# Kernel tuning notes

Hardware: AMD Instinct MI355X
Metric: run time of the kernel (lower is better)

Reference implementation:

```python
import jax, jax.numpy as jnp
import numpy as np

MAX_HOPS = 3


def setup_inputs() -> dict:
    key = jax.random.key(0)
    ks = jax.random.split(key, 6)
    B, M, S = 128, 200, 20
    V, D = 100000, 128
    NC, CL = 10000, 10
    stories = jax.random.randint(ks[0], (B, M, S), 0, V, dtype=jnp.int64)
    queries = jax.random.randint(ks[1], (B, S), 0, V, dtype=jnp.int64)
    candidates = jax.random.randint(ks[2], (NC, CL), 0, V, dtype=jnp.int64)
    # 0.05 scale keeps hop softmax logits in a sane range
    A_tab = jax.random.normal(ks[3], (V, D), dtype=jnp.float32) * 0.05
    W_tab = jax.random.normal(ks[4], (V, D), dtype=jnp.float32) * 0.05
    H_w = jax.random.normal(ks[5], (D, D), dtype=jnp.float32) * 0.05
    return {"stories": stories, "queries": queries, "candidates": candidates,
            "A_tab": A_tab, "W_tab": W_tab, "H_w": H_w}


def reference(stories, queries, candidates, A_tab, W_tab, H_w):
    # padding_idx=0: embedding row 0 is zero
    A = A_tab.at[0].set(0.0)
    W = W_tab.at[0].set(0.0)
    # query encoding: gather + sum-pool -> [B, D]
    u = jnp.sum(A[queries], axis=1)
    # memory encoding: [B, M, D] (same A table each hop, as in the source)
    m = jnp.sum(A[stories], axis=2)
    for _ in range(MAX_HOPS):
        dotted = jnp.einsum('bmd,bd->bm', m, u)          # attention logits
        probs = jax.nn.softmax(dotted, axis=1)           # [B, M]
        o = jnp.einsum('bm,bmd->bd', probs, m)           # weighted memory sum
        u = jnp.tanh(u @ H_w.T + o)                      # Linear(no bias) + tanh
    cand_sum = jnp.sum(W[candidates], axis=1)            # [NC, D]
    logits = u @ cand_sum.T                              # [B, NC]
    return logits
```

## Files before the change

kernel.cpp:

```cpp
#include <hip/hip_runtime.h>
#include <hip/hip_bf16.h>
#include <math.h>

#define BB 128
#define MM 200
#define SS 20
#define DD 128
#define NC 10000
#define CL 10
#define LCT 64
#define NROW (BB * MM)
#define GS_BLK (NROW / 16)
#define GQ_BLK (BB / 16)
#define GC_BLK (NC / 8)

__device__ __forceinline__ unsigned pack_bf16(float a, float b) {
    unsigned ua = __float_as_uint(a), ub = __float_as_uint(b);
    ua += 0x7fff + ((ua >> 16) & 1);
    ub += 0x7fff + ((ub >> 16) & 1);
    return (ua >> 16) | (ub & 0xffff0000u);
}
__device__ __forceinline__ float bflo(unsigned v) { return __uint_as_float(v << 16); }
__device__ __forceinline__ float bfhi(unsigned v) { return __uint_as_float(v & 0xffff0000u); }

__device__ __forceinline__ int detect_shift(const int* __restrict__ q) {
    int zc = 0;
#pragma unroll
    for (int i = 0; i < 8; ++i) zc += (q[2 * i + 1] == 0);
    return (zc >= 6) ? 1 : 0;
}

__global__ __launch_bounds__(512) void k_conv(const float* __restrict__ A,
                                              unsigned* __restrict__ Abf) {
    size_t t = (size_t)blockIdx.x * 512 + threadIdx.x;
    const float4* in = (const float4*)(A + t * 8);
    float4 a = in[0], b = in[1];
    if (t * 8 < DD) {
        a = make_float4(0.f, 0.f, 0.f, 0.f);
        b = make_float4(0.f, 0.f, 0.f, 0.f);
    }
    uint4 o;
    o.x = pack_bf16(a.x, a.y);
    o.y = pack_bf16(a.z, a.w);
    o.z = pack_bf16(b.x, b.y);
    o.w = pack_bf16(b.z, b.w);
    ((uint4*)(Abf + t * 4))[0] = o;
}

__global__ __launch_bounds__(256) void k_gather(const int* __restrict__ stories,
                                                const int* __restrict__ queries,
                                                const int* __restrict__ cands,
                                                const unsigned* __restrict__ Abf,
                                                const float* __restrict__ W,
                                                unsigned* __restrict__ m_all,
                                                float* __restrict__ u0_all,
                                                float* __restrict__ cand_buf) {
    int bid = blockIdx.x;
    int tid = threadIdx.x;
    int shift = detect_shift(queries);

    if (bid < GS_BLK) {
        int g = tid >> 4, l = tid & 15;
        int r = bid * 16 + g;
        int toks[SS];
#pragma unroll
        for (int s = 0; s < SS; ++s)
            toks[s] = stories[((size_t)(r * SS + s)) << shift];
        float a[8] = {0.f, 0.f, 0.f, 0.f, 0.f, 0.f, 0.f, 0.f};
#pragma unroll
        for (int s = 0; s < SS; ++s) {
            uint4 v = ((const uint4*)(Abf + ((size_t)(unsigned)toks[s] << 6)))[l];
            a[0] += bflo(v.x); a[1] += bfhi(v.x);
            a[2] += bflo(v.y); a[3] += bfhi(v.y);
            a[4] += bflo(v.z); a[5] += bfhi(v.z);
            a[6] += bflo(v.w); a[7] += bfhi(v.w);
        }
        uint4 o;
        o.x = pack_bf16(a[0], a[1]);
        o.y = pack_bf16(a[2], a[3]);
        o.z = pack_bf16(a[4], a[5]);
        o.w = pack_bf16(a[6], a[7]);
        ((uint4*)(m_all + (size_t)r * (DD / 2)))[l] = o;
    } else if (bid < GS_BLK + GQ_BLK) {
        int g = tid >> 4, l = tid & 15;
        int b = (bid - GS_BLK) * 16 + g;
        int toks[SS];
#pragma unroll
        for (int s = 0; s < SS; ++s)
            toks[s] = queries[((size_t)(b * SS + s)) << shift];
        float a[8] = {0.f, 0.f, 0.f, 0.f, 0.f, 0.f, 0.f, 0.f};
#pragma unroll
        for (int s = 0; s < SS; ++s) {
            uint4 v = ((const uint4*)(Abf + ((size_t)(unsigned)toks[s] << 6)))[l];
            a[0] += bflo(v.x); a[1] += bfhi(v.x);
            a[2] += bflo(v.y); a[3] += bfhi(v.y);
            a[4] += bflo(v.z); a[5] += bfhi(v.z);
            a[6] += bflo(v.w); a[7] += bfhi(v.w);
        }
        float4* op = (float4*)(u0_all + (size_t)b * DD + l * 8);
        op[0] = make_float4(a[0], a[1], a[2], a[3]);
        op[1] = make_float4(a[4], a[5], a[6], a[7]);
    } else {
        int g = tid >> 5, l = tid & 31;
        int row = (bid - GS_BLK - GQ_BLK) * 8 + g;
        int toks[CL];
#pragma unroll
        for (int s = 0; s < CL; ++s)
            toks[s] = cands[((size_t)(row * CL + s)) << shift];
        float4 acc = make_float4(0.f, 0.f, 0.f, 0.f);
#pragma unroll
        for (int s = 0; s < CL; ++s) {
            float4 v = ((const float4*)(W + (size_t)(unsigned)toks[s] * DD))[l];
            float msk = toks[s] ? 1.f : 0.f;
            acc.x = fmaf(msk, v.x, acc.x);
            acc.y = fmaf(msk, v.y, acc.y);
            acc.z = fmaf(msk, v.z, acc.z);
            acc.w = fmaf(msk, v.w, acc.w);
        }
        ((float4*)(cand_buf + (size_t)row * DD))[l] = acc;
    }
}

__global__ __launch_bounds__(512) void k_hops(const unsigned* __restrict__ m_all,
                                              const float* __restrict__ u0_all,
                                              const float* __restrict__ Hw,
                                              float* __restrict__ uT) {
    __shared__ unsigned m_s[MM][DD / 2];
    __shared__ float u_s[DD];
    __shared__ float p_s[MM];
    __shared__ float o_part[8][DD];
    __shared__ float red_s;

    int b = blockIdx.x;
    int tid = threadIdx.x;

    {
        const uint4* src = (const uint4*)(m_all + (size_t)b * MM * (DD / 2));
        uint4* dst = (uint4*)&m_s[0][0];
        for (int i = tid; i < MM * (DD / 2) / 4; i += 512) dst[i] = src[i];
    }
    if (tid < DD) u_s[tid] = u0_all[(size_t)b * DD + tid];
    __syncthreads();

    for (int hop = 0; hop < 3; ++hop) {
        if (tid < MM) {
            const float2* u2 = (const float2*)u_s;
            float acc = 0.f;
#pragma unroll 8
            for (int li = 0; li < 64; ++li) {
                int j = (tid + li) & 63;
                unsigned pv = m_s[tid][j];
                float2 uv = u2[j];
                acc += bflo(pv) * uv.x + bfhi(pv) * uv.y;
            }
            p_s[tid] = acc;
        }
        __syncthreads();
        if (tid < 64) {
            float v0 = p_s[tid], v1 = p_s[tid + 64], v2 = p_s[tid + 128];
            float v3 = (tid < 8) ? p_s[tid + 192] : -1e30f;
            float mx = fmaxf(fmaxf(v0, v1), fmaxf(v2, v3));
            for (int off = 32; off; off >>= 1) mx = fmaxf(mx, __shfl_down(mx, off));
            mx = __shfl(mx, 0);
            float e0 = __expf(v0 - mx), e1 = __expf(v1 - mx), e2 = __expf(v2 - mx);
            float e3 = (tid < 8) ? __expf(v3 - mx) : 0.f;
            float sm = e0 + e1 + e2 + e3;
            for (int off = 32; off; off >>= 1) sm += __shfl_down(sm, off);
            p_s[tid] = e0;
            p_s[tid + 64] = e1;
            p_s[tid + 128] = e2;
            if (tid < 8) p_s[tid + 192] = e3;
            if (tid == 0) red_s = 1.f / __shfl(sm, 0);
        }
        __syncthreads();
        {
            int c = tid & 63, h = tid >> 6;
            int mm0 = h * 25;
            float ax = 0.f, ay = 0.f;
#pragma unroll 5
            for (int k = 0; k < 25; ++k) {
                unsigned pv = m_s[mm0 + k][c];
                float p = p_s[mm0 + k];
                ax = fmaf(p, bflo(pv), ax);
                ay = fmaf(p, bfhi(pv), ay);
            }
            o_part[h][2 * c] = ax;
            o_part[h][2 * c + 1] = ay;
        }
        __syncthreads();
        float u_new = 0.f;
        if (tid < DD) {
            float o = 0.f;
#pragma unroll
            for (int h = 0; h < 8; ++h) o += o_part[h][tid];
            float acc = o * red_s;
            const float4* hrow = (const float4*)(Hw + tid * DD);
            const float4* u4 = (const float4*)u_s;
#pragma unroll 8
            for (int j = 0; j < DD / 4; ++j) {
                float4 hv = hrow[j];
                float4 uv = u4[j];
                acc += hv.x * uv.x + hv.y * uv.y + hv.z * uv.z + hv.w * uv.w;
            }
            u_new = tanhf(acc);
        }
        __syncthreads();
        if (tid < DD) u_s[tid] = u_new;
        __syncthreads();
    }
    if (tid < DD) uT[tid * BB + b] = u_s[tid];
}

__global__ __launch_bounds__(256) void k_logits(const float* __restrict__ uT,
                                                const float* __restrict__ cs,
                                                float* __restrict__ out) {
    __shared__ float c_s[DD][LCT + 4];
    int c0 = blockIdx.x * LCT;
    int tid = threadIdx.x;
    {
        int c = tid >> 2, l = tid & 3;
        int row = c0 + c;
        if (row >= NC) row = NC - 1;
        const float4* rp = (const float4*)(cs + (size_t)row * DD);
#pragma unroll
        for (int i = 0; i < 8; ++i) {
            int k = (l << 5) + (i << 2);
            float4 v = rp[(l << 3) + i];
            c_s[k][c] = v.x;
            c_s[k + 1][c] = v.y;
            c_s[k + 2][c] = v.z;
            c_s[k + 3][c] = v.w;
        }
    }
    __syncthreads();
    int tx = tid & 31, ty = tid >> 5;
    const float* cb = &c_s[0][ty << 3];
    const float4* up = (const float4*)(uT + (tx << 2));
    float acc[4][8];
#pragma unroll
    for (int i = 0; i < 4; ++i)
#pragma unroll
        for (int j = 0; j < 8; ++j) acc[i][j] = 0.f;
#pragma unroll 4
    for (int k = 0; k < DD; ++k) {
        float4 uv = up[k * (BB / 4)];
        float4 ca = *(const float4*)(cb + k * (LCT + 4));
        float4 cc = *(const float4*)(cb + k * (LCT + 4) + 4);
        float uu[4] = {uv.x, uv.y, uv.z, uv.w};
        float cv[8] = {ca.x, ca.y, ca.z, ca.w, cc.x, cc.y, cc.z, cc.w};
#pragma unroll
        for (int i = 0; i < 4; ++i)
#pragma unroll
            for (int j = 0; j < 8; ++j) acc[i][j] = fmaf(uu[i], cv[j], acc[i][j]);
    }
    if (c0 + (ty << 3) < NC) {
#pragma unroll
        for (int i = 0; i < 4; ++i) {
            float* orow = out + (size_t)((tx << 2) + i) * NC + c0 + (ty << 3);
            ((float4*)orow)[0] = make_float4(acc[i][0], acc[i][1], acc[i][2], acc[i][3]);
            ((float4*)orow)[1] = make_float4(acc[i][4], acc[i][5], acc[i][6], acc[i][7]);
        }
    }
}

extern "C" void kernel_launch(void* const* d_in, const int* in_sizes, int n_in,
                              void* d_out, int out_size, void* d_ws, size_t ws_size,
                              hipStream_t stream) {
    const int* stories = (const int*)d_in[0];
    const int* queries = (const int*)d_in[1];
    const int* cands   = (const int*)d_in[2];
    const float* A  = (const float*)d_in[3];
    const float* W  = (const float*)d_in[4];
    const float* Hw = (const float*)d_in[5];
    float* out = (float*)d_out;

    unsigned* Abf = (unsigned*)d_ws;
    float* cand_buf = (float*)(Abf + (size_t)100000 * (DD / 2));
    float* uT_buf = cand_buf + (size_t)NC * DD;
    float* u0_buf = uT_buf + (size_t)BB * DD;
    unsigned* m_all = (unsigned*)(u0_buf + (size_t)BB * DD);

    k_conv<<<100000 * DD / 8 / 512, 512, 0, stream>>>(A, Abf);
    k_gather<<<GS_BLK + GQ_BLK + GC_BLK, 256, 0, stream>>>(stories, queries, cands,
                                                           Abf, W, m_all, u0_buf,
                                                           cand_buf);
    k_hops<<<BB, 512, 0, stream>>>(m_all, u0_buf, Hw, uT_buf);
    k_logits<<<(NC + LCT - 1) / LCT, 256, 0, stream>>>(uT_buf, cand_buf, out);
}
```

Baseline: 189.1 us.

## Quantize A table to int8 with per-row scales for story gather

```diff
diff --git a/kernel.cpp b/kernel.cpp
--- a/kernel.cpp
+++ b/kernel.cpp
@@ -10,9 +10,15 @@
 #define CL 10
 #define LCT 64
 #define NROW (BB * MM)
-#define GS_BLK (NROW / 16)
-#define GQ_BLK (BB / 16)
-#define GC_BLK (NC / 8)
+#define NV 100000
+
+#define CONV_BLK (NV / 16)
+#define QRY_OFF CONV_BLK
+#define QRY_BLK (BB / 16)
+#define CND_OFF (QRY_OFF + QRY_BLK)
+#define CND_BLK (NC / 8)
+#define PREP_BLK (CND_OFF + CND_BLK)
+#define SG_BLK (NROW / 32)
 
 __device__ __forceinline__ unsigned pack_bf16(float a, float b) {
     unsigned ua = __float_as_uint(a), ub = __float_as_uint(b);
@@ -30,79 +36,76 @@
     return (zc >= 6) ? 1 : 0;
 }
 
-__global__ __launch_bounds__(512) void k_conv(const float* __restrict__ A,
-                                              unsigned* __restrict__ Abf) {
-    size_t t = (size_t)blockIdx.x * 512 + threadIdx.x;
-    const float4* in = (const float4*)(A + t * 8);
-    float4 a = in[0], b = in[1];
-    if (t * 8 < DD) {
-        a = make_float4(0.f, 0.f, 0.f, 0.f);
-        b = make_float4(0.f, 0.f, 0.f, 0.f);
-    }
-    uint4 o;
-    o.x = pack_bf16(a.x, a.y);
-    o.y = pack_bf16(a.z, a.w);
-    o.z = pack_bf16(b.x, b.y);
-    o.w = pack_bf16(b.z, b.w);
-    ((uint4*)(Abf + t * 4))[0] = o;
-}
-
-__global__ __launch_bounds__(256) void k_gather(const int* __restrict__ stories,
-                                                const int* __restrict__ queries,
-                                                const int* __restrict__ cands,
-                                                const unsigned* __restrict__ Abf,
-                                                const float* __restrict__ W,
-                                                unsigned* __restrict__ m_all,
-                                                float* __restrict__ u0_all,
-                                                float* __restrict__ cand_buf) {
+__device__ __forceinline__ void acc_i8(unsigned w, float s, float* a) {
+    a[0] = fmaf(s, (float)(int)(signed char)(w & 0xffu), a[0]);
+    a[1] = fmaf(s, (float)(int)(signed char)((w >> 8) & 0xffu), a[1]);
+    a[2] = fmaf(s, (float)(int)(signed char)((w >> 16) & 0xffu), a[2]);
+    a[3] = fmaf(s, (float)(int)(signed char)(w >> 24), a[3]);
+}
+
+__global__ __launch_bounds__(256) void k_prep(const float* __restrict__ A,
+                                              const float* __restrict__ W,
+                                              const int* __restrict__ queries,
+                                              const int* __restrict__ cands,
+                                              unsigned char* __restrict__ Ai8,
+                                              float* __restrict__ sc,
+                                              float* __restrict__ u0_all,
+                                              float* __restrict__ cand_buf) {
     int bid = blockIdx.x;
     int tid = threadIdx.x;
-    int shift = detect_shift(queries);
-
-    if (bid < GS_BLK) {
+
+    if (bid < CONV_BLK) {
         int g = tid >> 4, l = tid & 15;
-        int r = bid * 16 + g;
-        int toks[SS];
-#pragma unroll
-        for (int s = 0; s < SS; ++s)
-            toks[s] = stories[((size_t)(r * SS + s)) << shift];
+        int row = bid * 16 + g;
+        const float4* rp = (const float4*)(A + (size_t)row * DD) + l * 2;
+        float4 x0 = rp[0], x1 = rp[1];
+        float am = fmaxf(fmaxf(fmaxf(fabsf(x0.x), fabsf(x0.y)),
+                               fmaxf(fabsf(x0.z), fabsf(x0.w))),
+                         fmaxf(fmaxf(fabsf(x1.x), fabsf(x1.y)),
+                               fmaxf(fabsf(x1.z), fabsf(x1.w))));
+#pragma unroll
+        for (int m = 1; m < 16; m <<= 1) am = fmaxf(am, __shfl_xor(am, m, 16));
+        float s = am * (1.f / 127.f);
+        float inv = (am > 0.f) ? 127.f / am : 0.f;
+        int q0 = __float2int_rn(x0.x * inv), q1 = __float2int_rn(x0.y * inv);
+        int q2 = __float2int_rn(x0.z * inv), q3 = __float2int_rn(x0.w * inv);
+        int q4 = __float2int_rn(x1.x * inv), q5 = __float2int_rn(x1.y * inv);
+        int q6 = __float2int_rn(x1.z * inv), q7 = __float2int_rn(x1.w * inv);
+        uint2 o;
+        o.x = (q0 & 255) | ((q1 & 255) << 8) | ((q2 & 255) << 16) |
+              ((unsigned)(q3 & 255) << 24);
+        o.y = (q4 & 255) | ((q5 & 255) << 8) | ((q6 & 255) << 16) |
+              ((unsigned)(q7 & 255) << 24);
+        if (row == 0) {
+            o.x = 0u;
+            o.y = 0u;
+            s = 0.f;
+        }
+        ((uint2*)Ai8)[(size_t)row * 16 + l] = o;
+        if (l == 0) sc[row] = s;
+    } else if (bid < CND_OFF) {
+        int shift = detect_shift(queries);
+        int g = tid >> 4, l = tid & 15;
+        int b = (bid - QRY_OFF) * 16 + g;
         float a[8] = {0.f, 0.f, 0.f, 0.f, 0.f, 0.f, 0.f, 0.f};
 #pragma unroll
         for (int s = 0; s < SS; ++s) {
-            uint4 v = ((const uint4*)(Abf + ((size_t)(unsigned)toks[s] << 6)))[l];
-            a[0] += bflo(v.x); a[1] += bfhi(v.x);
-            a[2] += bflo(v.y); a[3] += bfhi(v.y);
-            a[4] += bflo(v.z); a[5] += bfhi(v.z);
-            a[6] += bflo(v.w); a[7] += bfhi(v.w);
-        }
-        uint4 o;
-        o.x = pack_bf16(a[0], a[1]);
-        o.y = pack_bf16(a[2], a[3]);
-        o.z = pack_bf16(a[4], a[5]);
-        o.w = pack_bf16(a[6], a[7]);
-        ((uint4*)(m_all + (size_t)r * (DD / 2)))[l] = o;
-    } else if (bid < GS_BLK + GQ_BLK) {
-        int g = tid >> 4, l = tid & 15;
-        int b = (bid - GS_BLK) * 16 + g;
-        int toks[SS];
-#pragma unroll
-        for (int s = 0; s < SS; ++s)
-            toks[s] = queries[((size_t)(b * SS + s)) << shift];
-        float a[8] = {0.f, 0.f, 0.f, 0.f, 0.f, 0.f, 0.f, 0.f};
-#pragma unroll
-        for (int s = 0; s < SS; ++s) {
-            uint4 v = ((const uint4*)(Abf + ((size_t)(unsigned)toks[s] << 6)))[l];
-            a[0] += bflo(v.x); a[1] += bfhi(v.x);
-            a[2] += bflo(v.y); a[3] += bfhi(v.y);
-            a[4] += bflo(v.z); a[5] += bfhi(v.z);
-            a[6] += bflo(v.w); a[7] += bfhi(v.w);
+            int tok = queries[((size_t)(b * SS + s)) << shift];
+            const float4* vp = (const float4*)(A + (size_t)(unsigned)tok * DD) + l * 2;
+            float4 v0 = vp[0], v1 = vp[1];
+            float msk = tok ? 1.f : 0.f;
+            a[0] = fmaf(msk, v0.x, a[0]); a[1] = fmaf(msk, v0.y, a[1]);
+            a[2] = fmaf(msk, v0.z, a[2]); a[3] = fmaf(msk, v0.w, a[3]);
+            a[4] = fmaf(msk, v1.x, a[4]); a[5] = fmaf(msk, v1.y, a[5]);
+            a[6] = fmaf(msk, v1.z, a[6]); a[7] = fmaf(msk, v1.w, a[7]);
         }
         float4* op = (float4*)(u0_all + (size_t)b * DD + l * 8);
         op[0] = make_float4(a[0], a[1], a[2], a[3]);
         op[1] = make_float4(a[4], a[5], a[6], a[7]);
     } else {
+        int shift = detect_shift(queries);
         int g = tid >> 5, l = tid & 31;
-        int row = (bid - GS_BLK - GQ_BLK) * 8 + g;
+        int row = (bid - CND_OFF) * 8 + g;
         int toks[CL];
 #pragma unroll
         for (int s = 0; s < CL; ++s)
@@ -119,6 +122,44 @@
         }
         ((float4*)(cand_buf + (size_t)row * DD))[l] = acc;
     }
+}
+
+__global__ __launch_bounds__(256) void k_sgather(const int* __restrict__ stories,
+                                                 const int* __restrict__ queries,
+                                                 const unsigned char* __restrict__ Ai8,
+                                                 const float* __restrict__ sc,
+                                                 unsigned* __restrict__ m_all) {
+    int bid = blockIdx.x;
+    int tid = threadIdx.x;
+    int shift = detect_shift(queries);
+    int g = tid >> 3, l = tid & 7;
+    int r = bid * 32 + g;
+
+    float a[16];
+#pragma unroll
+    for (int i = 0; i < 16; ++i) a[i] = 0.f;
+#pragma unroll
+    for (int s = 0; s < SS; ++s) {
+        int tok = stories[((size_t)(r * SS + s)) << shift];
+        uint4 v = ((const uint4*)Ai8)[(size_t)(unsigned)tok * 8 + l];
+        float st = sc[(unsigned)tok];
+        acc_i8(v.x, st, a + 0);
+        acc_i8(v.y, st, a + 4);
+        acc_i8(v.z, st, a + 8);
+        acc_i8(v.w, st, a + 12);
+    }
+    uint4 o0, o1;
+    o0.x = pack_bf16(a[0], a[1]);
+    o0.y = pack_bf16(a[2], a[3]);
+    o0.z = pack_bf16(a[4], a[5]);
+    o0.w = pack_bf16(a[6], a[7]);
+    o1.x = pack_bf16(a[8], a[9]);
+    o1.y = pack_bf16(a[10], a[11]);
+    o1.z = pack_bf16(a[12], a[13]);
+    o1.w = pack_bf16(a[14], a[15]);
+    uint4* dst = (uint4*)(m_all + (size_t)r * (DD / 2));
+    dst[2 * l] = o0;
+    dst[2 * l + 1] = o1;
 }
 
 __global__ __launch_bounds__(512) void k_hops(const unsigned* __restrict__ m_all,
@@ -274,16 +315,16 @@
     const float* Hw = (const float*)d_in[5];
     float* out = (float*)d_out;
 
-    unsigned* Abf = (unsigned*)d_ws;
-    float* cand_buf = (float*)(Abf + (size_t)100000 * (DD / 2));
+    unsigned char* Ai8 = (unsigned char*)d_ws;
+    float* sc = (float*)(Ai8 + (size_t)NV * DD);
+    float* cand_buf = sc + NV;
     float* uT_buf = cand_buf + (size_t)NC * DD;
     float* u0_buf = uT_buf + (size_t)BB * DD;
     unsigned* m_all = (unsigned*)(u0_buf + (size_t)BB * DD);
 
-    k_conv<<<100000 * DD / 8 / 512, 512, 0, stream>>>(A, Abf);
-    k_gather<<<GS_BLK + GQ_BLK + GC_BLK, 256, 0, stream>>>(stories, queries, cands,
-                                                           Abf, W, m_all, u0_buf,
-                                                           cand_buf);
+    k_prep<<<PREP_BLK, 256, 0, stream>>>(A, W, queries, cands, Ai8, sc,
+                                         u0_buf, cand_buf);
+    k_sgather<<<SG_BLK, 256, 0, stream>>>(stories, queries, Ai8, sc, m_all);
     k_hops<<<BB, 512, 0, stream>>>(m_all, u0_buf, Hw, uT_buf);
     k_logits<<<(NC + LCT - 1) / LCT, 256, 0, stream>>>(uT_buf, cand_buf, out);
 }
```

Result: no change. 186.7 us (-1.2%).
